# Kernel tuning notes

Measured on AMD Instinct MI355X. Metric: run time of the kernel, lower is better.

## Reference

```python
import jax, jax.numpy as jnp
import numpy as np

D_MODEL = 768
N_HEADS = 4
N_POINTS = 4
PATCH = 16
IMG = 224
HF = IMG // PATCH  # 14
WF = IMG // PATCH  # 14
LQ = HF * WF       # 196 tokens
DH = D_MODEL // N_HEADS  # 192


def setup_inputs() -> dict:
    key = jax.random.key(0)
    ks = jax.random.split(key, 14)
    s = 0.02
    inp = {
        "x": jax.random.normal(ks[0], (4, 16, 3, IMG, IMG), dtype=jnp.float32),
        # patch-embed conv (Conv2d 3->768, k=16, s=16)
        "embed_w": s * jax.random.normal(ks[1], (D_MODEL, 3, PATCH, PATCH), dtype=jnp.float32),
        "embed_b": jnp.zeros((D_MODEL,), dtype=jnp.float32),
        # MSDeformAttn linears (nn.Linear stores W as [out, in]; y = x @ W.T + b)
        "value_w": s * jax.random.normal(ks[2], (D_MODEL, D_MODEL), dtype=jnp.float32),
        "value_b": jnp.zeros((D_MODEL,), dtype=jnp.float32),
        "off_w": s * jax.random.normal(ks[3], (N_HEADS * N_POINTS * 2, D_MODEL), dtype=jnp.float32),
        "off_b": s * jax.random.normal(ks[4], (N_HEADS * N_POINTS * 2,), dtype=jnp.float32),
        "aw_w": s * jax.random.normal(ks[5], (N_HEADS * N_POINTS, D_MODEL), dtype=jnp.float32),
        "aw_b": jnp.zeros((N_HEADS * N_POINTS,), dtype=jnp.float32),
        "outp_w": s * jax.random.normal(ks[6], (D_MODEL, D_MODEL), dtype=jnp.float32),
        "outp_b": jnp.zeros((D_MODEL,), dtype=jnp.float32),
        # final nn.Linear proj
        "proj_w": s * jax.random.normal(ks[7], (D_MODEL, D_MODEL), dtype=jnp.float32),
        "proj_b": jnp.zeros((D_MODEL,), dtype=jnp.float32),
    }
    return inp


def _patch_embed(x, w, b):
    # x: (N,3,H,W); non-overlapping 16x16 patches == Conv2d(3,D,16,16)
    N = x.shape[0]
    xh = x.reshape(N, 3, HF, PATCH, WF, PATCH)
    feat = jnp.einsum('nchpwq,dcpq->nhwd', xh, w) + b  # (N,HF,WF,D)
    return feat.reshape(N, LQ, D_MODEL)


def _ref_points():
    lin = jnp.linspace(0.0, 1.0, HF)
    gy, gx = jnp.meshgrid(lin, lin, indexing='ij')
    return jnp.stack([gx, gy], -1).reshape(LQ, 2)  # (Lq, 2) in [0,1], (x,y)


def _deform_attn_core(value, loc, attn):
    # value: (N, Lq, M, Dh); loc: (N, Lq, M, P, 2) normalized [0,1]; attn: (N, Lq, M, P)
    N = value.shape[0]
    # grid_sample align_corners=False: pixel = (2*loc-1 + 1)*S/2 - 0.5 = loc*S - 0.5
    px = loc[..., 0] * WF - 0.5
    py = loc[..., 1] * HF - 0.5
    x0 = jnp.floor(px).astype(jnp.int32)
    y0 = jnp.floor(py).astype(jnp.int32)
    x1, y1 = x0 + 1, y0 + 1
    wx1 = px - x0.astype(px.dtype)
    wy1 = py - y0.astype(py.dtype)
    wx0, wy0 = 1.0 - wx1, 1.0 - wy1

    valh = value.transpose(0, 2, 1, 3)  # (N, M, HW, Dh)

    def gather(ix, iy):
        valid = (ix >= 0) & (ix < WF) & (iy >= 0) & (iy < HF)  # zeros padding
        idx = jnp.clip(iy, 0, HF - 1) * WF + jnp.clip(ix, 0, WF - 1)
        idxm = idx.transpose(0, 2, 1, 3).reshape(N, N_HEADS, LQ * N_POINTS)
        g = jnp.take_along_axis(valh, idxm[..., None], axis=2)  # (N,M,Lq*P,Dh)
        g = g * valid.transpose(0, 2, 1, 3).reshape(N, N_HEADS, LQ * N_POINTS, 1)
        return g.reshape(N, N_HEADS, LQ, N_POINTS, DH)

    def w4(a, b):  # (N,Lq,M,P) -> (N,M,Lq,P,1)
        return (a * b).transpose(0, 2, 1, 3)[..., None]

    sampled = (w4(wx0, wy0) * gather(x0, y0) + w4(wx1, wy0) * gather(x1, y0)
               + w4(wx0, wy1) * gather(x0, y1) + w4(wx1, wy1) * gather(x1, y1))
    # weighted combine over points
    out = (sampled * attn.transpose(0, 2, 1, 3)[..., None]).sum(3)  # (N,M,Lq,Dh)
    return out.transpose(0, 2, 1, 3).reshape(N, LQ, D_MODEL)


def reference(x, embed_w, embed_b, value_w, value_b, off_w, off_b, aw_w, aw_b,
              outp_w, outp_b, proj_w, proj_b):
    B, T = x.shape[0], x.shape[1]
    N = B * T
    xi = x.reshape(N, 3, IMG, IMG)
    feat = _patch_embed(xi, embed_w, embed_b)  # (N, Lq, D)

    # MSDeformAttn (n_levels=1)
    value = (feat @ value_w.T + value_b).reshape(N, LQ, N_HEADS, DH)
    off = (feat @ off_w.T + off_b).reshape(N, LQ, N_HEADS, N_POINTS, 2)
    aw = (feat @ aw_w.T + aw_b).reshape(N, LQ, N_HEADS, N_POINTS)
    aw = jax.nn.softmax(aw, axis=-1)  # softmax over n_levels*n_points = 4

    ref = _ref_points()  # (Lq, 2)
    norm = jnp.array([WF, HF], dtype=feat.dtype)  # offset_normalizer = (W, H)
    loc = ref[None, :, None, None, :] + off / norm  # (N,Lq,M,P,2)

    out = _deform_attn_core(value, loc, aw)
    out = out @ outp_w.T + outp_b  # output_proj

    pooled = out.mean(axis=1)  # mean over tokens
    final = pooled @ proj_w.T + proj_b
    return final.reshape(B, T, D_MODEL)
```

## Files before the change

kernel.cpp:

```cpp
#include <hip/hip_runtime.h>
#include <hip/hip_bf16.h>


using bf16 = __bf16;
typedef bf16  bf16x8 __attribute__((ext_vector_type(8)));
typedef float f32x4  __attribute__((ext_vector_type(4)));

#define N_IMG   64
#define LQ      196
#define DM      768
#define NH      4
#define DH      192
#define NPT     4
#define M_ROWS  (N_IMG * LQ)
#define NCAT    896

#define OFF_A     ((size_t)0)
#define OFF_FEAT  (OFF_A    + 19267584)
#define OFF_WEMB  (OFF_FEAT + 19267584)
#define OFF_WCAT  (OFF_WEMB + 1179648)
#define OFF_BCAT  (OFF_WCAT + 1376256)
#define OFF_CATO  (OFF_BCAT + 4096)
#define OFF_CORE  (OFF_CATO + 44957696)
#define OFF_POOL  (OFF_CORE + 196608)

__device__ __forceinline__ void gload_lds16(const bf16* g, bf16* l) {
#if __has_builtin(__builtin_amdgcn_global_load_lds)
  __builtin_amdgcn_global_load_lds(
      (const __attribute__((address_space(1))) void*)g,
      (__attribute__((address_space(3))) void*)l, 16, 0, 0);
#else
  *(bf16x8*)l = *(const bf16x8*)g;
#endif
}

__global__ void prep_kernel(const float* __restrict__ embed_w,
                            const float* __restrict__ value_w,
                            const float* __restrict__ off_w,
                            const float* __restrict__ aw_w,
                            const float* __restrict__ value_b,
                            const float* __restrict__ off_b,
                            const float* __restrict__ aw_b,
                            bf16* __restrict__ Wemb, bf16* __restrict__ Wcat,
                            float* __restrict__ bcat, float* __restrict__ core) {
  int idx = blockIdx.x * 256 + threadIdx.x;
  if (idx < DM * DM) Wemb[idx] = (bf16)embed_w[idx];
  if (idx < NCAT * DM) {
    int r = idx / DM, k = idx - r * DM;
    float v = 0.f;
    if (r < 768)       v = value_w[idx];
    else if (r < 800)  v = off_w[(r - 768) * DM + k];
    else if (r < 816)  v = aw_w[(r - 800) * DM + k];
    Wcat[idx] = (bf16)v;
  }
  if (idx < NCAT) {
    float v = 0.f;
    if (idx < 768)      v = value_b[idx];
    else if (idx < 800) v = off_b[idx - 768];
    else if (idx < 816) v = aw_b[idx - 800];
    bcat[idx] = v;
  }
  if (idx < N_IMG * DM) core[idx] = 0.f;
}

__global__ void im2col_kernel(const float* __restrict__ x, bf16* __restrict__ A) {
  int t = blockIdx.x * 256 + threadIdx.x;
  if (t >= N_IMG * 3 * 224 * 14) return;
  int w    = t % 14;
  int rest = t / 14;
  int y    = rest % 224;
  int nc   = rest / 224;
  int c    = nc % 3;
  int n    = nc / 3;
  int h = y >> 4, p = y & 15;
  const float* src = x + (size_t)rest * 224 + w * 16;
  bf16* dst = A + (size_t)(n * LQ + h * 14 + w) * DM + c * 256 + p * 16;
#pragma unroll
  for (int q = 0; q < 16; q += 4) {
    float4 v = *(const float4*)(src + q);
    dst[q + 0] = (bf16)v.x; dst[q + 1] = (bf16)v.y;
    dst[q + 2] = (bf16)v.z; dst[q + 3] = (bf16)v.w;
  }
}

template <typename OutT>
__global__ void gemm_bt(const bf16* __restrict__ A, const bf16* __restrict__ B,
                        const float* __restrict__ bias, OutT* __restrict__ C,
                        int M, int N, int K) {
  __shared__ bf16 As[128 * 64];
  __shared__ bf16 Bs[128 * 64];

  const int tid  = threadIdx.x;
  const int wave = tid >> 6;
  const int lane = tid & 63;
  const int mBase = blockIdx.x * 128;
  const int nBase = blockIdx.y * 128;
  const int wm = wave & 1;
  const int wn = wave >> 1;
  const int quad = lane >> 4;
  const int r16  = lane & 15;

  const f32x4 zero = {0.f, 0.f, 0.f, 0.f};
  f32x4 acc[4][4];
#pragma unroll
  for (int mi = 0; mi < 4; ++mi)
#pragma unroll
    for (int ni = 0; ni < 4; ++ni) acc[mi][ni] = zero;

  const int srow = wave * 32 + (lane >> 3);
  const int scol = (lane & 7) * 8;
  const bf16* Ag = A + (size_t)(mBase + srow) * K + scol;
  const bf16* Bg = B + (size_t)(nBase + srow) * K + scol;
  bf16* Al = As + srow * 64 + scol;
  bf16* Bl = Bs + srow * 64 + scol;

  for (int kt = 0; kt < K; kt += 64) {
#pragma unroll
    for (int i = 0; i < 4; ++i) {
      gload_lds16(Ag + (size_t)(i * 8) * K + kt, Al + i * 8 * 64);
      gload_lds16(Bg + (size_t)(i * 8) * K + kt, Bl + i * 8 * 64);
    }
    __syncthreads();
#pragma unroll
    for (int kk = 0; kk < 64; kk += 32) {
      bf16x8 af[4], bfr[4];
#pragma unroll
      for (int mi = 0; mi < 4; ++mi)
        af[mi] = *(const bf16x8*)&As[(wm * 64 + mi * 16 + r16) * 64 + kk + quad * 8];
#pragma unroll
      for (int ni = 0; ni < 4; ++ni)
        bfr[ni] = *(const bf16x8*)&Bs[(wn * 64 + ni * 16 + r16) * 64 + kk + quad * 8];
#pragma unroll
      for (int mi = 0; mi < 4; ++mi)
#pragma unroll
        for (int ni = 0; ni < 4; ++ni)
          acc[mi][ni] = __builtin_amdgcn_mfma_f32_16x16x32_bf16(
              af[mi], bfr[ni], acc[mi][ni], 0, 0, 0);
    }
    __syncthreads();
  }

#pragma unroll
  for (int ni = 0; ni < 4; ++ni) {
    const int col = nBase + wn * 64 + ni * 16 + r16;
    const float bv = bias[col];
#pragma unroll
    for (int mi = 0; mi < 4; ++mi) {
      const int row0 = mBase + wm * 64 + mi * 16 + quad * 4;
#pragma unroll
      for (int rr = 0; rr < 4; ++rr) {
        float v = acc[mi][ni][rr] + bv;
        C[(size_t)(row0 + rr) * N + col] = (OutT)v;
      }
    }
  }
}

__global__ void deform_kernel(const float* __restrict__ catout,
                              float* __restrict__ core) {
  __shared__ float s_w[64][4];
  __shared__ int   s_t[64][4];

  const int n   = blockIdx.x;
  const int lq0 = blockIdx.y * 4;
  const int z   = blockIdx.z;
  const int tid = threadIdx.x;
  const float* base = catout + (size_t)n * LQ * NCAT;

  if (tid < 64) {
    const int i = tid >> 4;
    const int m = (tid >> 2) & 3;
    const int p = tid & 3;
    const int lq = lq0 + i;
    const float* row = base + (size_t)lq * NCAT;

    const float l0 = row[800 + m * 4 + 0];
    const float l1 = row[800 + m * 4 + 1];
    const float l2 = row[800 + m * 4 + 2];
    const float l3 = row[800 + m * 4 + 3];
    const float mx = fmaxf(fmaxf(l0, l1), fmaxf(l2, l3));
    const float e0 = __expf(l0 - mx), e1 = __expf(l1 - mx);
    const float e2 = __expf(l2 - mx), e3 = __expf(l3 - mx);
    const float inv = 1.f / (e0 + e1 + e2 + e3);
    const float ep[4] = {e0, e1, e2, e3};
    const float ew = ep[p] * inv;

    const int h = lq / 14, w = lq - (lq / 14) * 14;
    const float px = (float)w * (14.f / 13.f) - 0.5f + row[768 + (m * 4 + p) * 2 + 0];
    const float py = (float)h * (14.f / 13.f) - 0.5f + row[768 + (m * 4 + p) * 2 + 1];
    const float fx = floorf(px), fy = floorf(py);
    const int x0 = (int)fx, y0 = (int)fy;
    const float wx1 = px - fx, wy1 = py - fy;
    const float wx0 = 1.f - wx1, wy0 = 1.f - wy1;

    const bool vx0 = (x0 >= 0) & (x0 < 14);
    const bool vx1 = (x0 >= -1) & (x0 < 13);
    const bool vy0 = (y0 >= 0) & (y0 < 14);
    const bool vy1 = (y0 >= -1) & (y0 < 13);
    const int cx0 = min(max(x0, 0), 13),     cx1 = min(max(x0 + 1, 0), 13);
    const int cy0 = min(max(y0, 0), 13) * 14, cy1 = min(max(y0 + 1, 0), 13) * 14;

    s_w[tid][0] = (vx0 & vy0) ? ew * wx0 * wy0 : 0.f;
    s_w[tid][1] = (vx1 & vy0) ? ew * wx1 * wy0 : 0.f;
    s_w[tid][2] = (vx0 & vy1) ? ew * wx0 * wy1 : 0.f;
    s_w[tid][3] = (vx1 & vy1) ? ew * wx1 * wy1 : 0.f;
    s_t[tid][0] = cy0 + cx0;
    s_t[tid][1] = cy0 + cx1;
    s_t[tid][2] = cy1 + cx0;
    s_t[tid][3] = cy1 + cx1;
  }
  __syncthreads();

  const int ch = z * 256 + tid;
  const int m  = ch / DH;
  float acc = 0.f;
#pragma unroll
  for (int i = 0; i < 4; ++i) {
#pragma unroll
    for (int p = 0; p < 4; ++p) {
      const int e = i * 16 + m * 4 + p;
      const float4 w4 = *(const float4*)s_w[e];
      const int4   t4 = *(const int4*)s_t[e];
      acc += w4.x * base[(size_t)(t4.x * NCAT + ch)];
      acc += w4.y * base[(size_t)(t4.y * NCAT + ch)];
      acc += w4.z * base[(size_t)(t4.z * NCAT + ch)];
      acc += w4.w * base[(size_t)(t4.w * NCAT + ch)];
    }
  }
  atomicAdd(&core[(size_t)n * DM + ch], acc * (1.f / 196.f));
}

__global__ void small_linear(const float* __restrict__ in,
                             const float* __restrict__ W,
                             const float* __restrict__ b,
                             float* __restrict__ out) {
  const int n = blockIdx.x;
  const int d = blockIdx.y * 256 + threadIdx.x;
  const float4* a4 = (const float4*)(in + (size_t)n * DM);
  const float4* w4 = (const float4*)(W + (size_t)d * DM);
  float acc = 0.f;
#pragma unroll 4
  for (int k = 0; k < DM / 4; ++k) {
    float4 a = a4[k], w = w4[k];
    acc += a.x * w.x + a.y * w.y + a.z * w.z + a.w * w.w;
  }
  out[(size_t)n * DM + d] = acc + b[d];
}

extern "C" void kernel_launch(void* const* d_in, const int* in_sizes, int n_in,
                              void* d_out, int out_size, void* d_ws, size_t ws_size,
                              hipStream_t stream) {
  const float* x       = (const float*)d_in[0];
  const float* embed_w = (const float*)d_in[1];
  const float* embed_b = (const float*)d_in[2];
  const float* value_w = (const float*)d_in[3];
  const float* value_b = (const float*)d_in[4];
  const float* off_w   = (const float*)d_in[5];
  const float* off_b   = (const float*)d_in[6];
  const float* aw_w    = (const float*)d_in[7];
  const float* aw_b    = (const float*)d_in[8];
  const float* outp_w  = (const float*)d_in[9];
  const float* outp_b  = (const float*)d_in[10];
  const float* proj_w  = (const float*)d_in[11];
  const float* proj_b  = (const float*)d_in[12];
  float* out = (float*)d_out;

  char* ws = (char*)d_ws;
  bf16*  A      = (bf16*)(ws + OFF_A);
  bf16*  feat   = (bf16*)(ws + OFF_FEAT);
  bf16*  Wemb   = (bf16*)(ws + OFF_WEMB);
  bf16*  Wcat   = (bf16*)(ws + OFF_WCAT);
  float* bcat   = (float*)(ws + OFF_BCAT);
  float* catout = (float*)(ws + OFF_CATO);
  float* core   = (float*)(ws + OFF_CORE);
  float* pooled = (float*)(ws + OFF_POOL);

  prep_kernel<<<dim3(2688), dim3(256), 0, stream>>>(
      embed_w, value_w, off_w, aw_w, value_b, off_b, aw_b, Wemb, Wcat, bcat, core);

  im2col_kernel<<<dim3(2352), dim3(256), 0, stream>>>(x, A);

  gemm_bt<bf16><<<dim3(M_ROWS / 128, DM / 128), dim3(256), 0, stream>>>(
      A, Wemb, embed_b, feat, M_ROWS, DM, DM);

  gemm_bt<float><<<dim3(M_ROWS / 128, NCAT / 128), dim3(256), 0, stream>>>(
      feat, Wcat, bcat, catout, M_ROWS, NCAT, DM);

  deform_kernel<<<dim3(N_IMG, 49, 3), dim3(256), 0, stream>>>(catout, core);

  small_linear<<<dim3(N_IMG, 3), dim3(256), 0, stream>>>(core, outp_w, outp_b, pooled);
  small_linear<<<dim3(N_IMG, 3), dim3(256), 0, stream>>>(pooled, proj_w, proj_b, out);
}
```

Before: 248.4 us.

## Split value/offset GEMM output into bf16 value buffer and compact fp32 offsets

The second GEMM now writes the 768 value channels as bf16 into a dedicated buffer and the offset and attention logits as fp32 into a compact 64-wide buffer, instead of a 896-wide fp32 concatenated output. The deform kernel reads these smaller buffers, roughly halving the bytes written and gathered for values. im2col is folded into the weight-prep kernel, removing one launch. The GEMM grid is also swapped so N tiles vary fastest, which is meant to improve A-tile reuse in cache. Values are rounded to bf16 before bilinear sampling, which adds a small precision loss.

```diff
diff --git a/kernel.cpp b/kernel.cpp
--- a/kernel.cpp
+++ b/kernel.cpp
@@ -11,7 +11,6 @@
 #define DM      768
 #define NH      4
 #define DH      192
-#define NPT     4
 #define M_ROWS  (N_IMG * LQ)
 #define NCAT    896
 
@@ -20,8 +19,9 @@
 #define OFF_WEMB  (OFF_FEAT + 19267584)
 #define OFF_WCAT  (OFF_WEMB + 1179648)
 #define OFF_BCAT  (OFF_WCAT + 1376256)
-#define OFF_CATO  (OFF_BCAT + 4096)
-#define OFF_CORE  (OFF_CATO + 44957696)
+#define OFF_VBUF  (OFF_BCAT + 4096)
+#define OFF_OA    (OFF_VBUF + 19267584)
+#define OFF_CORE  (OFF_OA   + 3211264)
 #define OFF_POOL  (OFF_CORE + 196608)
 
 __device__ __forceinline__ void gload_lds16(const bf16* g, bf16* l) {
@@ -34,23 +34,45 @@
 #endif
 }
 
-__global__ void prep_kernel(const float* __restrict__ embed_w,
-                            const float* __restrict__ value_w,
-                            const float* __restrict__ off_w,
-                            const float* __restrict__ aw_w,
-                            const float* __restrict__ value_b,
-                            const float* __restrict__ off_b,
-                            const float* __restrict__ aw_b,
-                            bf16* __restrict__ Wemb, bf16* __restrict__ Wcat,
-                            float* __restrict__ bcat, float* __restrict__ core) {
-  int idx = blockIdx.x * 256 + threadIdx.x;
+__global__ void stage_kernel(const float* __restrict__ x,
+                             const float* __restrict__ embed_w,
+                             const float* __restrict__ value_w,
+                             const float* __restrict__ off_w,
+                             const float* __restrict__ aw_w,
+                             const float* __restrict__ value_b,
+                             const float* __restrict__ off_b,
+                             const float* __restrict__ aw_b,
+                             bf16* __restrict__ A,
+                             bf16* __restrict__ Wemb, bf16* __restrict__ Wcat,
+                             float* __restrict__ bcat, float* __restrict__ core) {
+  const int bid = blockIdx.x;
+  if (bid < 9408) {
+    const int t   = bid * 256 + threadIdx.x;
+    const int row = t / 192;
+    const int j   = t - row * 192;
+    const int k   = j * 4;
+    const int c   = k >> 8;
+    const int r   = k & 255;
+    const int p   = r >> 4;
+    const int q   = r & 15;
+    const int n   = row / 196;
+    const int lq  = row - n * 196;
+    const int h   = lq / 14;
+    const int w   = lq - h * 14;
+    const float4 v = *(const float4*)(x +
+        ((((size_t)n * 3 + c) * 224) + h * 16 + p) * 224 + w * 16 + q);
+    bf16* dst = A + (size_t)row * DM + k;
+    dst[0] = (bf16)v.x; dst[1] = (bf16)v.y; dst[2] = (bf16)v.z; dst[3] = (bf16)v.w;
+    return;
+  }
+  const int idx = (bid - 9408) * 256 + threadIdx.x;
   if (idx < DM * DM) Wemb[idx] = (bf16)embed_w[idx];
-  if (idx < NCAT * DM) {
-    int r = idx / DM, k = idx - r * DM;
+  {
+    int rr = idx / DM, kk = idx - rr * DM;
     float v = 0.f;
-    if (r < 768)       v = value_w[idx];
-    else if (r < 800)  v = off_w[(r - 768) * DM + k];
-    else if (r < 816)  v = aw_w[(r - 800) * DM + k];
+    if (rr < 768)       v = value_w[idx];
+    else if (rr < 800)  v = off_w[(rr - 768) * DM + kk];
+    else if (rr < 816)  v = aw_w[(rr - 800) * DM + kk];
     Wcat[idx] = (bf16)v;
   }
   if (idx < NCAT) {
@@ -63,26 +85,6 @@
   if (idx < N_IMG * DM) core[idx] = 0.f;
 }
 
-__global__ void im2col_kernel(const float* __restrict__ x, bf16* __restrict__ A) {
-  int t = blockIdx.x * 256 + threadIdx.x;
-  if (t >= N_IMG * 3 * 224 * 14) return;
-  int w    = t % 14;
-  int rest = t / 14;
-  int y    = rest % 224;
-  int nc   = rest / 224;
-  int c    = nc % 3;
-  int n    = nc / 3;
-  int h = y >> 4, p = y & 15;
-  const float* src = x + (size_t)rest * 224 + w * 16;
-  bf16* dst = A + (size_t)(n * LQ + h * 14 + w) * DM + c * 256 + p * 16;
-#pragma unroll
-  for (int q = 0; q < 16; q += 4) {
-    float4 v = *(const float4*)(src + q);
-    dst[q + 0] = (bf16)v.x; dst[q + 1] = (bf16)v.y;
-    dst[q + 2] = (bf16)v.z; dst[q + 3] = (bf16)v.w;
-  }
-}
-
 template <typename OutT>
 __global__ void gemm_bt(const bf16* __restrict__ A, const bf16* __restrict__ B,
                         const float* __restrict__ bias, OutT* __restrict__ C,
@@ -93,8 +95,8 @@
   const int tid  = threadIdx.x;
   const int wave = tid >> 6;
   const int lane = tid & 63;
-  const int mBase = blockIdx.x * 128;
-  const int nBase = blockIdx.y * 128;
+  const int nBase = blockIdx.x * 128;
+  const int mBase = blockIdx.y * 128;
   const int wm = wave & 1;
   const int wn = wave >> 1;
   const int quad = lane >> 4;
@@ -156,7 +158,86 @@
   }
 }
 
-__global__ void deform_kernel(const float* __restrict__ catout,
+__global__ void gemm2_mixed(const bf16* __restrict__ A, const bf16* __restrict__ B,
+                            const float* __restrict__ bias,
+                            bf16* __restrict__ Vb, float* __restrict__ OA,
+                            int M, int N, int K) {
+  __shared__ bf16 As[128 * 64];
+  __shared__ bf16 Bs[128 * 64];
+
+  const int tid  = threadIdx.x;
+  const int wave = tid >> 6;
+  const int lane = tid & 63;
+  const int nBase = blockIdx.x * 128;
+  const int mBase = blockIdx.y * 128;
+  const int wm = wave & 1;
+  const int wn = wave >> 1;
+  const int quad = lane >> 4;
+  const int r16  = lane & 15;
+
+  const f32x4 zero = {0.f, 0.f, 0.f, 0.f};
+  f32x4 acc[4][4];
+#pragma unroll
+  for (int mi = 0; mi < 4; ++mi)
+#pragma unroll
+    for (int ni = 0; ni < 4; ++ni) acc[mi][ni] = zero;
+
+  const int srow = wave * 32 + (lane >> 3);
+  const int scol = (lane & 7) * 8;
+  const bf16* Ag = A + (size_t)(mBase + srow) * K + scol;
+  const bf16* Bg = B + (size_t)(nBase + srow) * K + scol;
+  bf16* Al = As + srow * 64 + scol;
+  bf16* Bl = Bs + srow * 64 + scol;
+
+  for (int kt = 0; kt < K; kt += 64) {
+#pragma unroll
+    for (int i = 0; i < 4; ++i) {
+      gload_lds16(Ag + (size_t)(i * 8) * K + kt, Al + i * 8 * 64);
+      gload_lds16(Bg + (size_t)(i * 8) * K + kt, Bl + i * 8 * 64);
+    }
+    __syncthreads();
+#pragma unroll
+    for (int kk = 0; kk < 64; kk += 32) {
+      bf16x8 af[4], bfr[4];
+#pragma unroll
+      for (int mi = 0; mi < 4; ++mi)
+        af[mi] = *(const bf16x8*)&As[(wm * 64 + mi * 16 + r16) * 64 + kk + quad * 8];
+#pragma unroll
+      for (int ni = 0; ni < 4; ++ni)
+        bfr[ni] = *(const bf16x8*)&Bs[(wn * 64 + ni * 16 + r16) * 64 + kk + quad * 8];
+#pragma unroll
+      for (int mi = 0; mi < 4; ++mi)
+#pragma unroll
+        for (int ni = 0; ni < 4; ++ni)
+          acc[mi][ni] = __builtin_amdgcn_mfma_f32_16x16x32_bf16(
+              af[mi], bfr[ni], acc[mi][ni], 0, 0, 0);
+    }
+    __syncthreads();
+  }
+
+#pragma unroll
+  for (int ni = 0; ni < 4; ++ni) {
+    const int col = nBase + wn * 64 + ni * 16 + r16;
+    const float bv = bias[col];
+#pragma unroll
+    for (int mi = 0; mi < 4; ++mi) {
+      const int row0 = mBase + wm * 64 + mi * 16 + quad * 4;
+#pragma unroll
+      for (int rr = 0; rr < 4; ++rr) {
+        float v = acc[mi][ni][rr] + bv;
+        int row = row0 + rr;
+        if (col < 768) {
+          Vb[(size_t)row * 768 + col] = (bf16)v;
+        } else if (col < 816) {
+          OA[(size_t)row * 64 + (col - 768)] = v;
+        }
+      }
+    }
+  }
+}
+
+__global__ void deform_kernel(const bf16* __restrict__ Vb,
+                              const float* __restrict__ OA,
                               float* __restrict__ core) {
   __shared__ float s_w[64][4];
   __shared__ int   s_t[64][4];
@@ -165,19 +246,18 @@
   const int lq0 = blockIdx.y * 4;
   const int z   = blockIdx.z;
   const int tid = threadIdx.x;
-  const float* base = catout + (size_t)n * LQ * NCAT;
 
   if (tid < 64) {
     const int i = tid >> 4;
     const int m = (tid >> 2) & 3;
     const int p = tid & 3;
     const int lq = lq0 + i;
-    const float* row = base + (size_t)lq * NCAT;
-
-    const float l0 = row[800 + m * 4 + 0];
-    const float l1 = row[800 + m * 4 + 1];
-    const float l2 = row[800 + m * 4 + 2];
-    const float l3 = row[800 + m * 4 + 3];
+    const float* row = OA + ((size_t)n * LQ + lq) * 64;
+
+    const float l0 = row[32 + m * 4 + 0];
+    const float l1 = row[32 + m * 4 + 1];
+    const float l2 = row[32 + m * 4 + 2];
+    const float l3 = row[32 + m * 4 + 3];
     const float mx = fmaxf(fmaxf(l0, l1), fmaxf(l2, l3));
     const float e0 = __expf(l0 - mx), e1 = __expf(l1 - mx);
     const float e2 = __expf(l2 - mx), e3 = __expf(l3 - mx);
@@ -186,8 +266,8 @@
     const float ew = ep[p] * inv;
 
     const int h = lq / 14, w = lq - (lq / 14) * 14;
-    const float px = (float)w * (14.f / 13.f) - 0.5f + row[768 + (m * 4 + p) * 2 + 0];
-    const float py = (float)h * (14.f / 13.f) - 0.5f + row[768 + (m * 4 + p) * 2 + 1];
+    const float px = (float)w * (14.f / 13.f) - 0.5f + row[(m * 4 + p) * 2 + 0];
+    const float py = (float)h * (14.f / 13.f) - 0.5f + row[(m * 4 + p) * 2 + 1];
     const float fx = floorf(px), fy = floorf(py);
     const int x0 = (int)fx, y0 = (int)fy;
     const float wx1 = px - fx, wy1 = py - fy;
@@ -197,7 +277,7 @@
     const bool vx1 = (x0 >= -1) & (x0 < 13);
     const bool vy0 = (y0 >= 0) & (y0 < 14);
     const bool vy1 = (y0 >= -1) & (y0 < 13);
-    const int cx0 = min(max(x0, 0), 13),     cx1 = min(max(x0 + 1, 0), 13);
+    const int cx0 = min(max(x0, 0), 13),      cx1 = min(max(x0 + 1, 0), 13);
     const int cy0 = min(max(y0, 0), 13) * 14, cy1 = min(max(y0 + 1, 0), 13) * 14;
 
     s_w[tid][0] = (vx0 & vy0) ? ew * wx0 * wy0 : 0.f;
@@ -213,6 +293,7 @@
 
   const int ch = z * 256 + tid;
   const int m  = ch / DH;
+  const bf16* vb = Vb + (size_t)n * LQ * 768 + ch;
   float acc = 0.f;
 #pragma unroll
   for (int i = 0; i < 4; ++i) {
@@ -221,10 +302,10 @@
       const int e = i * 16 + m * 4 + p;
       const float4 w4 = *(const float4*)s_w[e];
       const int4   t4 = *(const int4*)s_t[e];
-      acc += w4.x * base[(size_t)(t4.x * NCAT + ch)];
-      acc += w4.y * base[(size_t)(t4.y * NCAT + ch)];
-      acc += w4.z * base[(size_t)(t4.z * NCAT + ch)];
-      acc += w4.w * base[(size_t)(t4.w * NCAT + ch)];
+      acc += w4.x * (float)vb[(size_t)t4.x * 768];
+      acc += w4.y * (float)vb[(size_t)t4.y * 768];
+      acc += w4.z * (float)vb[(size_t)t4.z * 768];
+      acc += w4.w * (float)vb[(size_t)t4.w * 768];
     }
   }
   atomicAdd(&core[(size_t)n * DM + ch], acc * (1.f / 196.f));
@@ -271,22 +352,22 @@
   bf16*  Wemb   = (bf16*)(ws + OFF_WEMB);
   bf16*  Wcat   = (bf16*)(ws + OFF_WCAT);
   float* bcat   = (float*)(ws + OFF_BCAT);
-  float* catout = (float*)(ws + OFF_CATO);
+  bf16*  Vbuf   = (bf16*)(ws + OFF_VBUF);
+  float* OA     = (float*)(ws + OFF_OA);
   float* core   = (float*)(ws + OFF_CORE);
   float* pooled = (float*)(ws + OFF_POOL);
 
-  prep_kernel<<<dim3(2688), dim3(256), 0, stream>>>(
-      embed_w, value_w, off_w, aw_w, value_b, off_b, aw_b, Wemb, Wcat, bcat, core);
-
-  im2col_kernel<<<dim3(2352), dim3(256), 0, stream>>>(x, A);
-
-  gemm_bt<bf16><<<dim3(M_ROWS / 128, DM / 128), dim3(256), 0, stream>>>(
+  stage_kernel<<<dim3(12096), dim3(256), 0, stream>>>(
+      x, embed_w, value_w, off_w, aw_w, value_b, off_b, aw_b,
+      A, Wemb, Wcat, bcat, core);
+
+  gemm_bt<bf16><<<dim3(DM / 128, M_ROWS / 128), dim3(256), 0, stream>>>(
       A, Wemb, embed_b, feat, M_ROWS, DM, DM);
 
-  gemm_bt<float><<<dim3(M_ROWS / 128, NCAT / 128), dim3(256), 0, stream>>>(
-      feat, Wcat, bcat, catout, M_ROWS, NCAT, DM);
-
-  deform_kernel<<<dim3(N_IMG, 49, 3), dim3(256), 0, stream>>>(catout, core);
+  gemm2_mixed<<<dim3(NCAT / 128, M_ROWS / 128), dim3(256), 0, stream>>>(
+      feat, Wcat, bcat, Vbuf, OA, M_ROWS, NCAT, DM);
+
+  deform_kernel<<<dim3(N_IMG, 49, 3), dim3(256), 0, stream>>>(Vbuf, OA, core);
 
   small_linear<<<dim3(N_IMG, 3), dim3(256), 0, stream>>>(core, outp_w, outp_b, pooled);
   small_linear<<<dim3(N_IMG, 3), dim3(256), 0, stream>>>(pooled, proj_w, proj_b, out);
```

Measured after the change: 236.2 us. 1.05x faster.
